# Kernel optimization log

Hardware: AMD Instinct MI355X
Metric: run time of the kernel (lower is better)

Reference implementation:

```python
import jax, jax.numpy as jnp
import numpy as np
from jax import lax

B, N, C_IN = 16, 4096, 128
C_HID, N_CLS = 128, 10
DS = 32          # sparse_map_downsample
G = 4096 // DS   # quantized grid extent = 128


def setup_inputs() -> dict:
    key = jax.random.key(0)
    k = jax.random.split(key, 6)
    x = jax.random.normal(k[0], (B, N, C_IN), dtype=jnp.float32)
    coords = jax.random.randint(k[1], (B, N, 2), 0, 4096, dtype=jnp.int32)
    W1 = jax.random.normal(k[2], (3, 3, C_IN, C_HID), dtype=jnp.float32) * (1.0 / np.sqrt(9 * C_IN))
    W2 = jax.random.normal(k[3], (3, 3, C_HID, C_HID), dtype=jnp.float32) * (1.0 / np.sqrt(9 * C_HID))
    Wc = jax.random.normal(k[4], (C_HID, N_CLS), dtype=jnp.float32) * (1.0 / np.sqrt(C_HID))
    bc = jnp.zeros((N_CLS,), dtype=jnp.float32)
    return {"x": x, "coords": coords, "W1": W1, "W2": W2, "Wc": Wc, "bc": bc}


def reference(x, coords, W1, W2, Wc, bc):
    # --- coordinate quantization (tl / downsample, floored to int) ---
    q = jnp.floor(coords.astype(jnp.float32) / DS).astype(jnp.int32)  # [B,N,2] in [0,G)
    lin = q[..., 0] * G + q[..., 1]                                   # [B,N]
    seg = (jnp.arange(B, dtype=jnp.int32)[:, None] * (G * G) + lin).reshape(-1)  # [B*N]

    # --- UNWEIGHTED_AVERAGE quantization: average features colliding in a cell ---
    feats = x.reshape(-1, C_IN)
    sums = jax.ops.segment_sum(feats, seg, num_segments=B * G * G)            # [B*G*G, C]
    counts = jax.ops.segment_sum(jnp.ones((B * N,), x.dtype), seg, num_segments=B * G * G)
    grid = (sums / jnp.maximum(counts, 1.0)[:, None]).reshape(B, G, G, C_IN)  # dense sparse-map
    mask = (counts > 0).astype(x.dtype).reshape(B, G, G, 1)                   # occupancy

    # --- two sparse 3x3 convs (stride 1, no bias) + ReLU; outputs live only at
    #     occupied coordinates, so mask after each conv ---
    def sconv(g, W):
        y = lax.conv_general_dilated(g, W, window_strides=(1, 1), padding='SAME',
                                     dimension_numbers=('NHWC', 'HWIO', 'NHWC'))
        return jax.nn.relu(y) * mask

    h = sconv(grid, W1)
    h = sconv(h, W2)

    # --- MinkowskiGlobalAvgPooling: mean over occupied coordinates per bag ---
    npts = jnp.sum(mask, axis=(1, 2))            # [B,1]
    pooled = jnp.sum(h, axis=(1, 2)) / npts      # [B,C_HID]

    # --- MinkowskiLinear classifier ---
    logits = pooled @ Wc + bc                    # [B,N_CLS]
    return logits
```

## Files before the change

kernel.cpp:

```cpp
#include <hip/hip_runtime.h>
#include <hip/hip_bf16.h>

#define GG 16384
#define NBAG 16
#define NPT 65536
#define NCELL (NBAG * GG)
#define MAXM NPT
#define ZROW MAXM

typedef __bf16 bf16x8 __attribute__((ext_vector_type(8)));
typedef float f32x4 __attribute__((ext_vector_type(4)));

__global__ __launch_bounds__(256) void k_zero(float* __restrict__ fsum,
                                              int* __restrict__ counts,
                                              float* __restrict__ pooled) {
  int tid = blockIdx.x * 256 + threadIdx.x;
  int4 z = make_int4(0, 0, 0, 0);
#pragma unroll
  for (int i = 0; i < 4; ++i) ((int4*)fsum)[tid + i * 524288] = z;
  if (tid < 65536) ((int4*)counts)[tid] = z;
  if (tid < 512) ((int4*)pooled)[tid] = z;
}

__global__ __launch_bounds__(256) void k_setup(const float* __restrict__ W1,
                                               const float* __restrict__ W2,
                                               __hip_bfloat16* __restrict__ Wt1,
                                               __hip_bfloat16* __restrict__ Wt2,
                                               const int* __restrict__ coords,
                                               int* __restrict__ counts) {
  int b = blockIdx.x, t = threadIdx.x;
  if (b < 1152) {
    int id = b * 256 + t;
    const float* W = (id < 147456) ? W1 : W2;
    __hip_bfloat16* Wt = (id < 147456) ? Wt1 : Wt2;
    int r = (id < 147456) ? id : id - 147456;
    int k = r >> 14, rem = r & 16383, co = rem >> 7, ci = rem & 127;
    int dst = k * 16384 + co * 128 + (((ci >> 3) ^ (co & 7)) << 3) + (ci & 7);
    Wt[dst] = __float2bfloat16(W[k * 16384 + ci * 128 + co]);
  } else {
    int p = (b - 1152) * 256 + t;
    int bg = p >> 12;
    int q0 = coords[p * 2 + 0] >> 5;
    int q1 = coords[p * 2 + 1] >> 5;
    atomicAdd(&counts[bg * GG + q0 * 128 + q1], 1);
  }
}

__global__ __launch_bounds__(256) void k_s1(const int* __restrict__ counts,
                                            int* __restrict__ blockcnt) {
  __shared__ int red[256];
  int t = threadIdx.x;
  int base = blockIdx.x * 1024 + t * 4;
  int c = 0;
#pragma unroll
  for (int i = 0; i < 4; ++i) c += (counts[base + i] > 0) ? 1 : 0;
  red[t] = c;
  __syncthreads();
  for (int d = 128; d > 0; d >>= 1) {
    if (t < d) red[t] += red[t + d];
    __syncthreads();
  }
  if (t == 0) blockcnt[blockIdx.x] = red[0];
}

__global__ __launch_bounds__(256) void k_s2(const int* __restrict__ blockcnt,
                                            int* __restrict__ blockoff,
                                            int* __restrict__ dM,
                                            int* __restrict__ npts) {
  __shared__ int s[256];
  int t = threadIdx.x;
  int v = blockcnt[t];
  s[t] = v;
  __syncthreads();
  for (int d = 1; d < 256; d <<= 1) {
    int x = (t >= d) ? s[t - d] : 0;
    __syncthreads();
    s[t] += x;
    __syncthreads();
  }
  blockoff[t] = s[t] - v;
  if (t == 255) *dM = s[255];
  if (t < NBAG) {
    int sum = 0;
    for (int i = 0; i < 16; ++i) sum += blockcnt[t * 16 + i];
    npts[t] = sum;
  }
}

__global__ __launch_bounds__(256) void k_s3(const int* __restrict__ counts,
                                            const int* __restrict__ blockoff,
                                            int* __restrict__ cellidx,
                                            int* __restrict__ cell_of_idx) {
  __shared__ int s[256];
  int t = threadIdx.x;
  int base = blockIdx.x * 1024 + t * 4;
  int occ[4];
  int c = 0;
#pragma unroll
  for (int i = 0; i < 4; ++i) {
    occ[i] = counts[base + i] > 0;
    c += occ[i];
  }
  s[t] = c;
  __syncthreads();
  for (int d = 1; d < 256; d <<= 1) {
    int x = (t >= d) ? s[t - d] : 0;
    __syncthreads();
    s[t] += x;
    __syncthreads();
  }
  int pos = blockoff[blockIdx.x] + s[t] - c;
#pragma unroll
  for (int i = 0; i < 4; ++i) {
    if (occ[i]) {
      cellidx[base + i] = pos;
      cell_of_idx[pos] = base + i;
      pos++;
    } else {
      cellidx[base + i] = -1;
    }
  }
}

__global__ __launch_bounds__(256) void k_scatter(const float* __restrict__ x,
                                                 const int* __restrict__ coords,
                                                 const int* __restrict__ cellidx,
                                                 const int* __restrict__ counts,
                                                 float* __restrict__ fsum,
                                                 __hip_bfloat16* __restrict__ feat0) {
  int gid = blockIdx.x * 256 + threadIdx.x;
  int p = gid >> 7, c = gid & 127;
  int b = p >> 12;
  int q0 = coords[p * 2 + 0] >> 5;
  int q1 = coords[p * 2 + 1] >> 5;
  int cell = b * GG + q0 * 128 + q1;
  int idx = cellidx[cell];
  float v = x[(size_t)p * 128 + c];
  if (counts[cell] == 1) {
    feat0[(size_t)idx * 128 + c] = __float2bfloat16(v);
  } else {
    atomicAdd(&fsum[(size_t)idx * 128 + c], v);
  }
}

__global__ __launch_bounds__(256) void k_prep(const float* __restrict__ fsum,
                                              const int* __restrict__ counts,
                                              const int* __restrict__ cell_of_idx,
                                              const int* __restrict__ cellidx,
                                              const int* __restrict__ dM,
                                              __hip_bfloat16* __restrict__ feat0,
                                              __hip_bfloat16* __restrict__ feat1,
                                              int* __restrict__ nbrt) {
  int t = threadIdx.x;
  if (blockIdx.x < 4097) {
    int gid = blockIdx.x * 256 + t;
    int cell = gid >> 4, i = gid & 15;
    int M = *dM;
    if (cell >= M) {
      if (cell == M) {
        *(int4*)((char*)(feat0 + (size_t)ZROW * 128) + i * 16) = make_int4(0, 0, 0, 0);
      } else if (cell == M + 1) {
        *(int4*)((char*)(feat1 + (size_t)ZROW * 128) + i * 16) = make_int4(0, 0, 0, 0);
      }
      return;
    }
    int cnt = counts[cell_of_idx[cell]];
    if (cnt == 1) return;
    float inv = 1.0f / (float)cnt;
    const float4* src = (const float4*)fsum + (size_t)cell * 32 + i * 2;
    float4 v0 = src[0], v1 = src[1];
    __align__(16) __hip_bfloat16 h[8];
    h[0] = __float2bfloat16(v0.x * inv);
    h[1] = __float2bfloat16(v0.y * inv);
    h[2] = __float2bfloat16(v0.z * inv);
    h[3] = __float2bfloat16(v0.w * inv);
    h[4] = __float2bfloat16(v1.x * inv);
    h[5] = __float2bfloat16(v1.y * inv);
    h[6] = __float2bfloat16(v1.z * inv);
    h[7] = __float2bfloat16(v1.w * inv);
    *(int4*)(feat0 + (size_t)cell * 128 + i * 8) = *(const int4*)h;
  } else {
    int idx = (blockIdx.x - 4097) * 256 + t;
    if (idx >= MAXM) return;
    if (idx >= *dM) {
#pragma unroll
      for (int j = 0; j < 9; ++j) nbrt[j * MAXM + idx] = ZROW;
      return;
    }
    int cell = cell_of_idx[idx];
    int b = cell >> 14, ij = cell & 16383;
    int i = ij >> 7, j = ij & 127;
#pragma unroll
    for (int dh = 0; dh < 3; ++dh)
#pragma unroll
      for (int dw = 0; dw < 3; ++dw) {
        int ni = i + dh - 1, nj = j + dw - 1;
        int v = -1;
        if (ni >= 0 && ni < 128 && nj >= 0 && nj < 128)
          v = cellidx[b * GG + ni * 128 + nj];
        nbrt[(dh * 3 + dw) * MAXM + idx] = (v < 0) ? ZROW : v;
      }
  }
}

template <bool POOL>
__global__ __launch_bounds__(256, 2) void k_conv(
    const __hip_bfloat16* __restrict__ fin,
    const __hip_bfloat16* __restrict__ Wt,
    __hip_bfloat16* __restrict__ fout,
    float* __restrict__ pooled,
    const int* __restrict__ nbrt,
    const int* __restrict__ cell_of_idx,
    const int* __restrict__ dM) {
  __shared__ __align__(16) char smem[65536];
  const int M = *dM;
  const int lb = (blockIdx.x & 7) * (gridDim.x >> 3) + (blockIdx.x >> 3);
  const int base = lb * 128;
  if (base >= M) return;
  const int t = threadIdx.x;
  const int w = t >> 6;
  const int l = t & 63;
  const int u = l >> 4;
  const int c = l & 15;
  const int wrow = base + w * 32;

  auto stageW = [&](int k, int b) {
    const __hip_bfloat16* gw = Wt + (size_t)k * 16384 + w * 4096;
    char* lbuf = smem + b * 32768 + w * 8192;
#pragma unroll
    for (int j = 0; j < 8; ++j) {
      __builtin_amdgcn_global_load_lds(
          (const __attribute__((address_space(1))) void*)(gw + j * 512 + l * 8),
          (__attribute__((address_space(3))) void*)(lbuf + j * 1024), 16, 0, 0);
    }
  };
  auto loadA = [&](int nb, int kb) {
    return *(const bf16x8*)((const char*)fin + (size_t)nb * 256 + kb * 64 + u * 16);
  };

  f32x4 acc[2][8];
#pragma unroll
  for (int mf = 0; mf < 2; ++mf)
#pragma unroll
    for (int nf = 0; nf < 8; ++nf) acc[mf][nf] = f32x4{0.f, 0.f, 0.f, 0.f};

  bf16x8 aP[2][2][4];
  int nb_c[2], nb_n[2];
  nb_c[0] = nbrt[0 * MAXM + wrow + c];
  nb_c[1] = nbrt[0 * MAXM + wrow + 16 + c];
  nb_n[0] = nbrt[1 * MAXM + wrow + c];
  nb_n[1] = nbrt[1 * MAXM + wrow + 16 + c];
#pragma unroll
  for (int mf = 0; mf < 2; ++mf)
#pragma unroll
    for (int kb = 0; kb < 4; ++kb) aP[0][mf][kb] = loadA(nb_c[mf], kb);
  stageW(0, 0);
  __syncthreads();

#pragma unroll
  for (int k = 0; k < 9; ++k) {
    const int cp = k & 1, np = cp ^ 1;
    if (k < 8) {
#pragma unroll
      for (int mf = 0; mf < 2; ++mf)
#pragma unroll
        for (int kb = 0; kb < 4; ++kb) aP[np][mf][kb] = loadA(nb_n[mf], kb);
      stageW(k + 1, (k + 1) & 1);
    }
    if (k < 7) {
      nb_n[0] = nbrt[(k + 2) * MAXM + wrow + c];
      nb_n[1] = nbrt[(k + 2) * MAXM + wrow + 16 + c];
    }
    const char* wb = smem + (k & 1) * 32768;
    __builtin_amdgcn_s_setprio(1);
#pragma unroll
    for (int kb = 0; kb < 4; ++kb) {
      bf16x8 wf[8];
#pragma unroll
      for (int nf = 0; nf < 8; ++nf) {
        int co = nf * 16 + c;
        int ch = (kb * 4 + u) ^ (c & 7);
        wf[nf] = *(const bf16x8*)(wb + co * 256 + ch * 16);
      }
#pragma unroll
      for (int mf = 0; mf < 2; ++mf)
#pragma unroll
        for (int nf = 0; nf < 8; ++nf)
          acc[mf][nf] = __builtin_amdgcn_mfma_f32_16x16x32_bf16(
              aP[cp][mf][kb], wf[nf], acc[mf][nf], 0, 0, 0);
    }
    __builtin_amdgcn_s_setprio(0);
    __syncthreads();
  }

  if (!POOL) {
    char* ep = smem + w * 8704;
#pragma unroll
    for (int mf = 0; mf < 2; ++mf)
#pragma unroll
      for (int nf = 0; nf < 8; ++nf)
#pragma unroll
        for (int i = 0; i < 4; ++i) {
          int rl = mf * 16 + u * 4 + i;
          int col = nf * 16 + c;
          *(__hip_bfloat16*)(ep + rl * 272 + col * 2) =
              __float2bfloat16(fmaxf(acc[mf][nf][i], 0.f));
        }
    __syncthreads();
#pragma unroll
    for (int j = 0; j < 8; ++j) {
      int rl = j * 4 + u;
      int grow = wrow + rl;
      int4 v = *(const int4*)(ep + rl * 272 + c * 16);
      if (grow < M)
        *(int4*)((char*)fout + (size_t)grow * 256 + c * 16) = v;
    }
  } else {
    if (wrow < M) {
      int b0 = cell_of_idx[wrow] >> 14;
      int lastr = min(wrow + 31, M - 1);
      int b1 = cell_of_idx[lastr] >> 14;
      float p0[8] = {0.f, 0.f, 0.f, 0.f, 0.f, 0.f, 0.f, 0.f};
      float p1[8] = {0.f, 0.f, 0.f, 0.f, 0.f, 0.f, 0.f, 0.f};
#pragma unroll
      for (int mf = 0; mf < 2; ++mf)
#pragma unroll
        for (int i = 0; i < 4; ++i) {
          int r = wrow + mf * 16 + u * 4 + i;
          int bg = (r < M) ? (cell_of_idx[r] >> 14) : -1;
#pragma unroll
          for (int nf = 0; nf < 8; ++nf) {
            float v = fmaxf(acc[mf][nf][i], 0.f);
            if (bg == b0) p0[nf] += v;
            else if (bg == b1) p1[nf] += v;
          }
        }
      bool two = (b1 != b0);
#pragma unroll
      for (int nf = 0; nf < 8; ++nf) {
        p0[nf] += __shfl_xor(p0[nf], 16);
        p0[nf] += __shfl_xor(p0[nf], 32);
        p1[nf] += __shfl_xor(p1[nf], 16);
        p1[nf] += __shfl_xor(p1[nf], 32);
      }
      if (u == 0) {
#pragma unroll
        for (int nf = 0; nf < 8; ++nf) {
          atomicAdd(&pooled[b0 * 128 + nf * 16 + c], p0[nf]);
          if (two) atomicAdd(&pooled[b1 * 128 + nf * 16 + c], p1[nf]);
        }
      }
    }
  }
}

__global__ __launch_bounds__(256) void k_logits(const float* __restrict__ pooled,
                                                const int* __restrict__ npts,
                                                const float* __restrict__ Wc,
                                                const float* __restrict__ bc,
                                                float* __restrict__ out) {
  int t = threadIdx.x;
  if (t >= 160) return;
  int b = t / 10, n = t % 10;
  float inv = 1.0f / (float)npts[b];
  float s = 0.f;
  for (int c = 0; c < 128; ++c) s += pooled[b * 128 + c] * Wc[c * 10 + n];
  out[t] = s * inv + bc[n];
}

extern "C" void kernel_launch(void* const* d_in, const int* in_sizes, int n_in,
                              void* d_out, int out_size, void* d_ws, size_t ws_size,
                              hipStream_t stream) {
  const float* x = (const float*)d_in[0];
  const int* coords = (const int*)d_in[1];
  const float* W1 = (const float*)d_in[2];
  const float* W2 = (const float*)d_in[3];
  const float* Wc = (const float*)d_in[4];
  const float* bc = (const float*)d_in[5];
  float* out = (float*)d_out;

  char* ws = (char*)d_ws;
  size_t off = 0;
  auto take = [&](size_t bytes) {
    void* p = ws + off;
    off += (bytes + 255) & ~(size_t)255;
    return p;
  };
  int* counts      = (int*)take((size_t)NCELL * 4);
  int* cellidx     = (int*)take((size_t)NCELL * 4);
  int* cell_of_idx = (int*)take((size_t)MAXM * 4);
  int* blockcnt    = (int*)take(256 * 4);
  int* blockoff    = (int*)take(256 * 4);
  int* dM          = (int*)take(4);
  int* npts        = (int*)take(64);
  int* nbrt        = (int*)take((size_t)9 * MAXM * 4);
  float* fsum      = (float*)take((size_t)MAXM * 128 * 4);
  __hip_bfloat16* feat0 = (__hip_bfloat16*)take((size_t)(MAXM + 1) * 128 * 2);
  __hip_bfloat16* feat1 = (__hip_bfloat16*)take((size_t)(MAXM + 1) * 128 * 2);
  __hip_bfloat16* Wt1   = (__hip_bfloat16*)take((size_t)9 * 128 * 128 * 2);
  __hip_bfloat16* Wt2   = (__hip_bfloat16*)take((size_t)9 * 128 * 128 * 2);
  float* pooled    = (float*)take(16 * 128 * 4);

  k_zero<<<2048, 256, 0, stream>>>(fsum, counts, pooled);
  k_setup<<<1408, 256, 0, stream>>>(W1, W2, Wt1, Wt2, coords, counts);
  k_s1<<<256, 256, 0, stream>>>(counts, blockcnt);
  k_s2<<<1, 256, 0, stream>>>(blockcnt, blockoff, dM, npts);
  k_s3<<<256, 256, 0, stream>>>(counts, blockoff, cellidx, cell_of_idx);
  k_scatter<<<NPT * 128 / 256, 256, 0, stream>>>(x, coords, cellidx, counts, fsum, feat0);
  k_prep<<<4353, 256, 0, stream>>>(fsum, counts, cell_of_idx, cellidx, dM, feat0, feat1, nbrt);
  k_conv<false><<<MAXM / 128, 256, 0, stream>>>(feat0, Wt1, feat1, nullptr, nbrt, cell_of_idx, dM);
  k_conv<true><<<MAXM / 128, 256, 0, stream>>>(feat1, Wt2, nullptr, pooled, nbrt, cell_of_idx, dM);
  k_logits<<<1, 256, 0, stream>>>(pooled, npts, Wc, bc, out);
}
```

Measured before the change: 108.5 us.

## Fuse scan and logits stages, zero fsum only for multi-point cells, vectorize scatter

Merges the two-kernel block scan into one kernel using a last-block-done atomic counter, and folds the logits computation into the tail of the pooling conv kernel the same way. It stops zeroing the full 32 MB fsum buffer and instead zeroes only the rows of cells holding more than one point, recording them in a list so the averaging pass touches only those rows. The scatter now moves float4s per thread and the neighbor table build is fused with it. These changes cut launches and memory traffic, at the cost of atomic counters and threadfence-based cross-block signalling.

```diff
diff --git a/kernel.cpp b/kernel.cpp
--- a/kernel.cpp
+++ b/kernel.cpp
@@ -11,15 +11,20 @@
 typedef __bf16 bf16x8 __attribute__((ext_vector_type(8)));
 typedef float f32x4 __attribute__((ext_vector_type(4)));
 
-__global__ __launch_bounds__(256) void k_zero(float* __restrict__ fsum,
-                                              int* __restrict__ counts,
-                                              float* __restrict__ pooled) {
+__global__ __launch_bounds__(256) void k_zero(int* __restrict__ counts,
+                                              float* __restrict__ pooled,
+                                              int* __restrict__ dcnt,
+                                              __hip_bfloat16* __restrict__ feat0,
+                                              __hip_bfloat16* __restrict__ feat1) {
   int tid = blockIdx.x * 256 + threadIdx.x;
   int4 z = make_int4(0, 0, 0, 0);
-#pragma unroll
-  for (int i = 0; i < 4; ++i) ((int4*)fsum)[tid + i * 524288] = z;
-  if (tid < 65536) ((int4*)counts)[tid] = z;
+  ((int4*)counts)[tid] = z;
   if (tid < 512) ((int4*)pooled)[tid] = z;
+  if (tid == 513) { dcnt[0] = 0; dcnt[1] = 0; dcnt[2] = 0; dcnt[3] = 0; }
+  if (tid >= 1024 && tid < 1040)
+    ((int4*)(feat0 + (size_t)ZROW * 128))[tid - 1024] = z;
+  if (tid >= 1056 && tid < 1072)
+    ((int4*)(feat1 + (size_t)ZROW * 128))[tid - 1056] = z;
 }
 
 __global__ __launch_bounds__(256) void k_setup(const float* __restrict__ W1,
@@ -46,9 +51,14 @@
   }
 }
 
-__global__ __launch_bounds__(256) void k_s1(const int* __restrict__ counts,
-                                            int* __restrict__ blockcnt) {
+__global__ __launch_bounds__(256) void k_scan(const int* __restrict__ counts,
+                                              int* __restrict__ blockcnt,
+                                              int* __restrict__ blockoff,
+                                              int* __restrict__ dM,
+                                              int* __restrict__ npts,
+                                              int* __restrict__ dcnt) {
   __shared__ int red[256];
+  __shared__ int isLast;
   int t = threadIdx.x;
   int base = blockIdx.x * 1024 + t * 4;
   int c = 0;
@@ -60,26 +70,25 @@
     if (t < d) red[t] += red[t + d];
     __syncthreads();
   }
-  if (t == 0) blockcnt[blockIdx.x] = red[0];
-}
-
-__global__ __launch_bounds__(256) void k_s2(const int* __restrict__ blockcnt,
-                                            int* __restrict__ blockoff,
-                                            int* __restrict__ dM,
-                                            int* __restrict__ npts) {
-  __shared__ int s[256];
-  int t = threadIdx.x;
+  if (t == 0) {
+    blockcnt[blockIdx.x] = red[0];
+    __threadfence();
+    isLast = (atomicAdd(&dcnt[0], 1) == 255);
+  }
+  __syncthreads();
+  if (!isLast) return;
+  __threadfence();
   int v = blockcnt[t];
-  s[t] = v;
+  red[t] = v;
   __syncthreads();
   for (int d = 1; d < 256; d <<= 1) {
-    int x = (t >= d) ? s[t - d] : 0;
-    __syncthreads();
-    s[t] += x;
-    __syncthreads();
-  }
-  blockoff[t] = s[t] - v;
-  if (t == 255) *dM = s[255];
+    int x = (t >= d) ? red[t - d] : 0;
+    __syncthreads();
+    red[t] += x;
+    __syncthreads();
+  }
+  blockoff[t] = red[t] - v;
+  if (t == 255) *dM = red[255];
   if (t < NBAG) {
     int sum = 0;
     for (int i = 0; i < 16; ++i) sum += blockcnt[t * 16 + i];
@@ -90,7 +99,10 @@
 __global__ __launch_bounds__(256) void k_s3(const int* __restrict__ counts,
                                             const int* __restrict__ blockoff,
                                             int* __restrict__ cellidx,
-                                            int* __restrict__ cell_of_idx) {
+                                            int* __restrict__ cell_of_idx,
+                                            float* __restrict__ fsum,
+                                            int* __restrict__ mlist,
+                                            int* __restrict__ dcnt) {
   __shared__ int s[256];
   int t = threadIdx.x;
   int base = blockIdx.x * 1024 + t * 4;
@@ -110,11 +122,18 @@
     __syncthreads();
   }
   int pos = blockoff[blockIdx.x] + s[t] - c;
+  int4 z = make_int4(0, 0, 0, 0);
 #pragma unroll
   for (int i = 0; i < 4; ++i) {
     if (occ[i]) {
       cellidx[base + i] = pos;
       cell_of_idx[pos] = base + i;
+      if (counts[base + i] > 1) {
+        mlist[atomicAdd(&dcnt[1], 1)] = pos;
+        int4* fz = (int4*)(fsum + (size_t)pos * 128);
+#pragma unroll
+        for (int j = 0; j < 32; ++j) fz[j] = z;
+      }
       pos++;
     } else {
       cellidx[base + i] = -1;
@@ -122,52 +141,74 @@
   }
 }
 
-__global__ __launch_bounds__(256) void k_scatter(const float* __restrict__ x,
-                                                 const int* __restrict__ coords,
-                                                 const int* __restrict__ cellidx,
-                                                 const int* __restrict__ counts,
-                                                 float* __restrict__ fsum,
-                                                 __hip_bfloat16* __restrict__ feat0) {
-  int gid = blockIdx.x * 256 + threadIdx.x;
-  int p = gid >> 7, c = gid & 127;
-  int b = p >> 12;
-  int q0 = coords[p * 2 + 0] >> 5;
-  int q1 = coords[p * 2 + 1] >> 5;
-  int cell = b * GG + q0 * 128 + q1;
-  int idx = cellidx[cell];
-  float v = x[(size_t)p * 128 + c];
-  if (counts[cell] == 1) {
-    feat0[(size_t)idx * 128 + c] = __float2bfloat16(v);
+__global__ __launch_bounds__(256) void k_gather(const float* __restrict__ x,
+                                                const int* __restrict__ coords,
+                                                const int* __restrict__ cellidx,
+                                                const int* __restrict__ counts,
+                                                const int* __restrict__ cell_of_idx,
+                                                const int* __restrict__ dM,
+                                                float* __restrict__ fsum,
+                                                __hip_bfloat16* __restrict__ feat0,
+                                                int* __restrict__ nbrt) {
+  int b = blockIdx.x, t = threadIdx.x;
+  if (b < 8192) {
+    int gid = b * 256 + t;
+    int p = gid >> 5, c4 = gid & 31;
+    int bg = p >> 12;
+    int q0 = coords[p * 2 + 0] >> 5;
+    int q1 = coords[p * 2 + 1] >> 5;
+    int cell = bg * GG + q0 * 128 + q1;
+    int idx = cellidx[cell];
+    float4 v = ((const float4*)x)[(size_t)p * 32 + c4];
+    if (counts[cell] == 1) {
+      __align__(8) __hip_bfloat16 h[4];
+      h[0] = __float2bfloat16(v.x);
+      h[1] = __float2bfloat16(v.y);
+      h[2] = __float2bfloat16(v.z);
+      h[3] = __float2bfloat16(v.w);
+      *(int2*)(feat0 + (size_t)idx * 128 + c4 * 4) = *(const int2*)h;
+    } else {
+      float* dst = fsum + (size_t)idx * 128 + c4 * 4;
+      atomicAdd(dst + 0, v.x);
+      atomicAdd(dst + 1, v.y);
+      atomicAdd(dst + 2, v.z);
+      atomicAdd(dst + 3, v.w);
+    }
   } else {
-    atomicAdd(&fsum[(size_t)idx * 128 + c], v);
-  }
-}
-
-__global__ __launch_bounds__(256) void k_prep(const float* __restrict__ fsum,
-                                              const int* __restrict__ counts,
-                                              const int* __restrict__ cell_of_idx,
-                                              const int* __restrict__ cellidx,
-                                              const int* __restrict__ dM,
-                                              __hip_bfloat16* __restrict__ feat0,
-                                              __hip_bfloat16* __restrict__ feat1,
-                                              int* __restrict__ nbrt) {
-  int t = threadIdx.x;
-  if (blockIdx.x < 4097) {
-    int gid = blockIdx.x * 256 + t;
-    int cell = gid >> 4, i = gid & 15;
-    int M = *dM;
-    if (cell >= M) {
-      if (cell == M) {
-        *(int4*)((char*)(feat0 + (size_t)ZROW * 128) + i * 16) = make_int4(0, 0, 0, 0);
-      } else if (cell == M + 1) {
-        *(int4*)((char*)(feat1 + (size_t)ZROW * 128) + i * 16) = make_int4(0, 0, 0, 0);
-      }
+    int idx = (b - 8192) * 256 + t;
+    if (idx >= *dM) {
+#pragma unroll
+      for (int j = 0; j < 9; ++j) nbrt[j * MAXM + idx] = ZROW;
       return;
     }
-    int cnt = counts[cell_of_idx[cell]];
-    if (cnt == 1) return;
-    float inv = 1.0f / (float)cnt;
-    const float4* src = (const float4*)fsum + (size_t)cell * 32 + i * 2;
+    int cell = cell_of_idx[idx];
+    int bb = cell >> 14, ij = cell & 16383;
+    int i = ij >> 7, j = ij & 127;
+#pragma unroll
+    for (int dh = 0; dh < 3; ++dh)
+#pragma unroll
+      for (int dw = 0; dw < 3; ++dw) {
+        int ni = i + dh - 1, nj = j + dw - 1;
+        int v = -1;
+        if (ni >= 0 && ni < 128 && nj >= 0 && nj < 128)
+          v = cellidx[bb * GG + ni * 128 + nj];
+        nbrt[(dh * 3 + dw) * MAXM + idx] = (v < 0) ? ZROW : v;
+      }
+  }
+}
+
+__global__ __launch_bounds__(256) void k_avg(const float* __restrict__ fsum,
+                                             const int* __restrict__ counts,
+                                             const int* __restrict__ cell_of_idx,
+                                             const int* __restrict__ mlist,
+                                             const int* __restrict__ dcnt,
+                                             __hip_bfloat16* __restrict__ feat0) {
+  int total = dcnt[1] * 16;
+  for (int gid = blockIdx.x * 256 + threadIdx.x; gid < total; gid += 128 * 256) {
+    int e = gid >> 4, i = gid & 15;
+    int pos = mlist[e];
+    float inv = 1.0f / (float)counts[cell_of_idx[pos]];
+    const float4* src = (const float4*)fsum + (size_t)pos * 32 + i * 2;
     float4 v0 = src[0], v1 = src[1];
     __align__(16) __hip_bfloat16 h[8];
     h[0] = __float2bfloat16(v0.x * inv);
@@ -178,28 +219,7 @@
     h[5] = __float2bfloat16(v1.y * inv);
     h[6] = __float2bfloat16(v1.z * inv);
     h[7] = __float2bfloat16(v1.w * inv);
-    *(int4*)(feat0 + (size_t)cell * 128 + i * 8) = *(const int4*)h;
-  } else {
-    int idx = (blockIdx.x - 4097) * 256 + t;
-    if (idx >= MAXM) return;
-    if (idx >= *dM) {
-#pragma unroll
-      for (int j = 0; j < 9; ++j) nbrt[j * MAXM + idx] = ZROW;
-      return;
-    }
-    int cell = cell_of_idx[idx];
-    int b = cell >> 14, ij = cell & 16383;
-    int i = ij >> 7, j = ij & 127;
-#pragma unroll
-    for (int dh = 0; dh < 3; ++dh)
-#pragma unroll
-      for (int dw = 0; dw < 3; ++dw) {
-        int ni = i + dh - 1, nj = j + dw - 1;
-        int v = -1;
-        if (ni >= 0 && ni < 128 && nj >= 0 && nj < 128)
-          v = cellidx[b * GG + ni * 128 + nj];
-        nbrt[(dh * 3 + dw) * MAXM + idx] = (v < 0) ? ZROW : v;
-      }
+    *(int4*)(feat0 + (size_t)pos * 128 + i * 8) = *(const int4*)h;
   }
 }
 
@@ -211,161 +231,171 @@
     float* __restrict__ pooled,
     const int* __restrict__ nbrt,
     const int* __restrict__ cell_of_idx,
-    const int* __restrict__ dM) {
+    const int* __restrict__ dM,
+    const int* __restrict__ npts,
+    const float* __restrict__ Wc,
+    const float* __restrict__ bc,
+    float* __restrict__ out,
+    int* __restrict__ dcnt) {
   __shared__ __align__(16) char smem[65536];
+  __shared__ int lastb;
   const int M = *dM;
   const int lb = (blockIdx.x & 7) * (gridDim.x >> 3) + (blockIdx.x >> 3);
   const int base = lb * 128;
-  if (base >= M) return;
   const int t = threadIdx.x;
-  const int w = t >> 6;
-  const int l = t & 63;
-  const int u = l >> 4;
-  const int c = l & 15;
-  const int wrow = base + w * 32;
-
-  auto stageW = [&](int k, int b) {
-    const __hip_bfloat16* gw = Wt + (size_t)k * 16384 + w * 4096;
-    char* lbuf = smem + b * 32768 + w * 8192;
-#pragma unroll
-    for (int j = 0; j < 8; ++j) {
-      __builtin_amdgcn_global_load_lds(
-          (const __attribute__((address_space(1))) void*)(gw + j * 512 + l * 8),
-          (__attribute__((address_space(3))) void*)(lbuf + j * 1024), 16, 0, 0);
-    }
-  };
-  auto loadA = [&](int nb, int kb) {
-    return *(const bf16x8*)((const char*)fin + (size_t)nb * 256 + kb * 64 + u * 16);
-  };
-
-  f32x4 acc[2][8];
-#pragma unroll
-  for (int mf = 0; mf < 2; ++mf)
-#pragma unroll
-    for (int nf = 0; nf < 8; ++nf) acc[mf][nf] = f32x4{0.f, 0.f, 0.f, 0.f};
-
-  bf16x8 aP[2][2][4];
-  int nb_c[2], nb_n[2];
-  nb_c[0] = nbrt[0 * MAXM + wrow + c];
-  nb_c[1] = nbrt[0 * MAXM + wrow + 16 + c];
-  nb_n[0] = nbrt[1 * MAXM + wrow + c];
-  nb_n[1] = nbrt[1 * MAXM + wrow + 16 + c];
-#pragma unroll
-  for (int mf = 0; mf < 2; ++mf)
-#pragma unroll
-    for (int kb = 0; kb < 4; ++kb) aP[0][mf][kb] = loadA(nb_c[mf], kb);
-  stageW(0, 0);
-  __syncthreads();
-
-#pragma unroll
-  for (int k = 0; k < 9; ++k) {
-    const int cp = k & 1, np = cp ^ 1;
-    if (k < 8) {
+  if (!POOL && base >= M) return;
+  if (base < M) {
+    const int w = t >> 6;
+    const int l = t & 63;
+    const int u = l >> 4;
+    const int c = l & 15;
+    const int wrow = base + w * 32;
+
+    auto stageW = [&](int k, int b) {
+      const __hip_bfloat16* gw = Wt + (size_t)k * 16384 + w * 4096;
+      char* lbuf = smem + b * 32768 + w * 8192;
+#pragma unroll
+      for (int j = 0; j < 8; ++j) {
+        __builtin_amdgcn_global_load_lds(
+            (const __attribute__((address_space(1))) void*)(gw + j * 512 + l * 8),
+            (__attribute__((address_space(3))) void*)(lbuf + j * 1024), 16, 0, 0);
+      }
+    };
+    auto loadA = [&](int nb, int kb) {
+      return *(const bf16x8*)((const char*)fin + (size_t)nb * 256 + kb * 64 + u * 16);
+    };
+
+    f32x4 acc[2][8];
+#pragma unroll
+    for (int mf = 0; mf < 2; ++mf)
+#pragma unroll
+      for (int nf = 0; nf < 8; ++nf) acc[mf][nf] = f32x4{0.f, 0.f, 0.f, 0.f};
+
+    bf16x8 aP[2][2][4];
+    int nb_c[2], nb_n[2];
+    nb_c[0] = nbrt[0 * MAXM + wrow + c];
+    nb_c[1] = nbrt[0 * MAXM + wrow + 16 + c];
+    nb_n[0] = nbrt[1 * MAXM + wrow + c];
+    nb_n[1] = nbrt[1 * MAXM + wrow + 16 + c];
+#pragma unroll
+    for (int mf = 0; mf < 2; ++mf)
+#pragma unroll
+      for (int kb = 0; kb < 4; ++kb) aP[0][mf][kb] = loadA(nb_c[mf], kb);
+    stageW(0, 0);
+    __syncthreads();
+
+#pragma unroll
+    for (int k = 0; k < 9; ++k) {
+      const int cp = k & 1, np = cp ^ 1;
+      if (k < 8) {
+#pragma unroll
+        for (int mf = 0; mf < 2; ++mf)
+#pragma unroll
+          for (int kb = 0; kb < 4; ++kb) aP[np][mf][kb] = loadA(nb_n[mf], kb);
+        stageW(k + 1, (k + 1) & 1);
+      }
+      if (k < 7) {
+        nb_n[0] = nbrt[(k + 2) * MAXM + wrow + c];
+        nb_n[1] = nbrt[(k + 2) * MAXM + wrow + 16 + c];
+      }
+      const char* wb = smem + (k & 1) * 32768;
+      __builtin_amdgcn_s_setprio(1);
+#pragma unroll
+      for (int kb = 0; kb < 4; ++kb) {
+        bf16x8 wf[8];
+#pragma unroll
+        for (int nf = 0; nf < 8; ++nf) {
+          int co = nf * 16 + c;
+          int ch = (kb * 4 + u) ^ (c & 7);
+          wf[nf] = *(const bf16x8*)(wb + co * 256 + ch * 16);
+        }
+#pragma unroll
+        for (int mf = 0; mf < 2; ++mf)
+#pragma unroll
+          for (int nf = 0; nf < 8; ++nf)
+            acc[mf][nf] = __builtin_amdgcn_mfma_f32_16x16x32_bf16(
+                aP[cp][mf][kb], wf[nf], acc[mf][nf], 0, 0, 0);
+      }
+      __builtin_amdgcn_s_setprio(0);
+      __syncthreads();
+    }
+
+    if (!POOL) {
+      char* ep = smem + w * 8704;
 #pragma unroll
       for (int mf = 0; mf < 2; ++mf)
 #pragma unroll
-        for (int kb = 0; kb < 4; ++kb) aP[np][mf][kb] = loadA(nb_n[mf], kb);
-      stageW(k + 1, (k + 1) & 1);
-    }
-    if (k < 7) {
-      nb_n[0] = nbrt[(k + 2) * MAXM + wrow + c];
-      nb_n[1] = nbrt[(k + 2) * MAXM + wrow + 16 + c];
-    }
-    const char* wb = smem + (k & 1) * 32768;
-    __builtin_amdgcn_s_setprio(1);
-#pragma unroll
-    for (int kb = 0; kb < 4; ++kb) {
-      bf16x8 wf[8];
-#pragma unroll
-      for (int nf = 0; nf < 8; ++nf) {
-        int co = nf * 16 + c;
-        int ch = (kb * 4 + u) ^ (c & 7);
-        wf[nf] = *(const bf16x8*)(wb + co * 256 + ch * 16);
-      }
-#pragma unroll
-      for (int mf = 0; mf < 2; ++mf)
-#pragma unroll
         for (int nf = 0; nf < 8; ++nf)
-          acc[mf][nf] = __builtin_amdgcn_mfma_f32_16x16x32_bf16(
-              aP[cp][mf][kb], wf[nf], acc[mf][nf], 0, 0, 0);
-    }
-    __builtin_amdgcn_s_setprio(0);
-    __syncthreads();
-  }
-
-  if (!POOL) {
-    char* ep = smem + w * 8704;
-#pragma unroll
-    for (int mf = 0; mf < 2; ++mf)
-#pragma unroll
-      for (int nf = 0; nf < 8; ++nf)
-#pragma unroll
-        for (int i = 0; i < 4; ++i) {
-          int rl = mf * 16 + u * 4 + i;
-          int col = nf * 16 + c;
-          *(__hip_bfloat16*)(ep + rl * 272 + col * 2) =
-              __float2bfloat16(fmaxf(acc[mf][nf][i], 0.f));
+#pragma unroll
+          for (int i = 0; i < 4; ++i) {
+            int rl = mf * 16 + u * 4 + i;
+            int col = nf * 16 + c;
+            *(__hip_bfloat16*)(ep + rl * 272 + col * 2) =
+                __float2bfloat16(fmaxf(acc[mf][nf][i], 0.f));
+          }
+      __syncthreads();
+#pragma unroll
+      for (int j = 0; j < 8; ++j) {
+        int rl = j * 4 + u;
+        int grow = wrow + rl;
+        int4 v = *(const int4*)(ep + rl * 272 + c * 16);
+        if (grow < M)
+          *(int4*)((char*)fout + (size_t)grow * 256 + c * 16) = v;
+      }
+    } else {
+      if (wrow < M) {
+        int b0 = cell_of_idx[wrow] >> 14;
+        int lastr = min(wrow + 31, M - 1);
+        int b1 = cell_of_idx[lastr] >> 14;
+        float p0[8] = {0.f, 0.f, 0.f, 0.f, 0.f, 0.f, 0.f, 0.f};
+        float p1[8] = {0.f, 0.f, 0.f, 0.f, 0.f, 0.f, 0.f, 0.f};
+#pragma unroll
+        for (int mf = 0; mf < 2; ++mf)
+#pragma unroll
+          for (int i = 0; i < 4; ++i) {
+            int r = wrow + mf * 16 + u * 4 + i;
+            int bg = (r < M) ? (cell_of_idx[r] >> 14) : -1;
+#pragma unroll
+            for (int nf = 0; nf < 8; ++nf) {
+              float v = fmaxf(acc[mf][nf][i], 0.f);
+              if (bg == b0) p0[nf] += v;
+              else if (bg == b1) p1[nf] += v;
+            }
+          }
+        bool two = (b1 != b0);
+#pragma unroll
+        for (int nf = 0; nf < 8; ++nf) {
+          p0[nf] += __shfl_xor(p0[nf], 16);
+          p0[nf] += __shfl_xor(p0[nf], 32);
+          p1[nf] += __shfl_xor(p1[nf], 16);
+          p1[nf] += __shfl_xor(p1[nf], 32);
         }
-    __syncthreads();
-#pragma unroll
-    for (int j = 0; j < 8; ++j) {
-      int rl = j * 4 + u;
-      int grow = wrow + rl;
-      int4 v = *(const int4*)(ep + rl * 272 + c * 16);
-      if (grow < M)
-        *(int4*)((char*)fout + (size_t)grow * 256 + c * 16) = v;
-    }
-  } else {
-    if (wrow < M) {
-      int b0 = cell_of_idx[wrow] >> 14;
-      int lastr = min(wrow + 31, M - 1);
-      int b1 = cell_of_idx[lastr] >> 14;
-      float p0[8] = {0.f, 0.f, 0.f, 0.f, 0.f, 0.f, 0.f, 0.f};
-      float p1[8] = {0.f, 0.f, 0.f, 0.f, 0.f, 0.f, 0.f, 0.f};
-#pragma unroll
-      for (int mf = 0; mf < 2; ++mf)
-#pragma unroll
-        for (int i = 0; i < 4; ++i) {
-          int r = wrow + mf * 16 + u * 4 + i;
-          int bg = (r < M) ? (cell_of_idx[r] >> 14) : -1;
+        if (u == 0) {
 #pragma unroll
           for (int nf = 0; nf < 8; ++nf) {
-            float v = fmaxf(acc[mf][nf][i], 0.f);
-            if (bg == b0) p0[nf] += v;
-            else if (bg == b1) p1[nf] += v;
+            atomicAdd(&pooled[b0 * 128 + nf * 16 + c], p0[nf]);
+            if (two) atomicAdd(&pooled[b1 * 128 + nf * 16 + c], p1[nf]);
           }
         }
-      bool two = (b1 != b0);
-#pragma unroll
-      for (int nf = 0; nf < 8; ++nf) {
-        p0[nf] += __shfl_xor(p0[nf], 16);
-        p0[nf] += __shfl_xor(p0[nf], 32);
-        p1[nf] += __shfl_xor(p1[nf], 16);
-        p1[nf] += __shfl_xor(p1[nf], 32);
-      }
-      if (u == 0) {
-#pragma unroll
-        for (int nf = 0; nf < 8; ++nf) {
-          atomicAdd(&pooled[b0 * 128 + nf * 16 + c], p0[nf]);
-          if (two) atomicAdd(&pooled[b1 * 128 + nf * 16 + c], p1[nf]);
-        }
-      }
-    }
-  }
-}
-
-__global__ __launch_bounds__(256) void k_logits(const float* __restrict__ pooled,
-                                                const int* __restrict__ npts,
-                                                const float* __restrict__ Wc,
-                                                const float* __restrict__ bc,
-                                                float* __restrict__ out) {
-  int t = threadIdx.x;
-  if (t >= 160) return;
-  int b = t / 10, n = t % 10;
-  float inv = 1.0f / (float)npts[b];
-  float s = 0.f;
-  for (int c = 0; c < 128; ++c) s += pooled[b * 128 + c] * Wc[c * 10 + n];
-  out[t] = s * inv + bc[n];
+      }
+    }
+  }
+
+  if (POOL) {
+    __threadfence();
+    if (t == 0) lastb = (atomicAdd(&dcnt[2], 1) == (int)gridDim.x - 1);
+    __syncthreads();
+    if (lastb) {
+      __threadfence();
+      if (t < 160) {
+        int b = t / 10, n = t % 10;
+        float inv = 1.0f / (float)npts[b];
+        float s = 0.f;
+        for (int cc = 0; cc < 128; ++cc) s += pooled[b * 128 + cc] * Wc[cc * 10 + n];
+        out[t] = s * inv + bc[n];
+      }
+    }
+  }
 }
 
 extern "C" void kernel_launch(void* const* d_in, const int* in_sizes, int n_in,
@@ -393,6 +423,8 @@
   int* blockoff    = (int*)take(256 * 4);
   int* dM          = (int*)take(4);
   int* npts        = (int*)take(64);
+  int* dcnt        = (int*)take(64);
+  int* mlist       = (int*)take((size_t)MAXM * 4);
   int* nbrt        = (int*)take((size_t)9 * MAXM * 4);
   float* fsum      = (float*)take((size_t)MAXM * 128 * 4);
   __hip_bfloat16* feat0 = (__hip_bfloat16*)take((size_t)(MAXM + 1) * 128 * 2);
@@ -401,14 +433,15 @@
   __hip_bfloat16* Wt2   = (__hip_bfloat16*)take((size_t)9 * 128 * 128 * 2);
   float* pooled    = (float*)take(16 * 128 * 4);
 
-  k_zero<<<2048, 256, 0, stream>>>(fsum, counts, pooled);
+  k_zero<<<256, 256, 0, stream>>>(counts, pooled, dcnt, feat0, feat1);
   k_setup<<<1408, 256, 0, stream>>>(W1, W2, Wt1, Wt2, coords, counts);
-  k_s1<<<256, 256, 0, stream>>>(counts, blockcnt);
-  k_s2<<<1, 256, 0, stream>>>(blockcnt, blockoff, dM, npts);
-  k_s3<<<256, 256, 0, stream>>>(counts, blockoff, cellidx, cell_of_idx);
-  k_scatter<<<NPT * 128 / 256, 256, 0, stream>>>(x, coords, cellidx, counts, fsum, feat0);
-  k_prep<<<4353, 256, 0, stream>>>(fsum, counts, cell_of_idx, cellidx, dM, feat0, feat1, nbrt);
-  k_conv<false><<<MAXM / 128, 256, 0, stream>>>(feat0, Wt1, feat1, nullptr, nbrt, cell_of_idx, dM);
-  k_conv<true><<<MAXM / 128, 256, 0, stream>>>(feat1, Wt2, nullptr, pooled, nbrt, cell_of_idx, dM);
-  k_logits<<<1, 256, 0, stream>>>(pooled, npts, Wc, bc, out);
-}
+  k_scan<<<256, 256, 0, stream>>>(counts, blockcnt, blockoff, dM, npts, dcnt);
+  k_s3<<<256, 256, 0, stream>>>(counts, blockoff, cellidx, cell_of_idx, fsum, mlist, dcnt);
+  k_gather<<<8448, 256, 0, stream>>>(x, coords, cellidx, counts, cell_of_idx, dM,
+                                     fsum, feat0, nbrt);
+  k_avg<<<128, 256, 0, stream>>>(fsum, counts, cell_of_idx, mlist, dcnt, feat0);
+  k_conv<false><<<MAXM / 128, 256, 0, stream>>>(feat0, Wt1, feat1, nullptr, nbrt,
+                                                cell_of_idx, dM, npts, Wc, bc, out, dcnt);
+  k_conv<true><<<MAXM / 128, 256, 0, stream>>>(feat1, Wt2, nullptr, pooled, nbrt,
+                                               cell_of_idx, dM, npts, Wc, bc, out, dcnt);
+}
```

New measurement: 191.5 us. +76.5%, slower.
